# Optimization experiments

Hardware: AMD Instinct MI355X
Metric: run time of the kernel (lower is better)

Reference implementation:

```python
import jax, jax.numpy as jnp
import numpy as np

B, NIMG, H, W, C = 4, 4, 80, 80, 256
NH = 8
C1 = C // 8          # 32
CPH = C1 // NH       # 4 per-head conv channels
K2D = 4              # deformable attention sampling points
HD2 = C1 // NH       # 4 head dim for 2D deformable attention
INNER = 32           # 3D deformable attention inner dim
DSF = (2, 8, 8)
OSC = jnp.array([2.0, 8.0, 8.0], jnp.float32)


def _bilin2d(img, px, py):
    # img [B,C,H,W]; px,py [B,K] pixel coords -> [B,K,C], zero-padded outside
    Bb, Cc, Hh, Ww = img.shape
    x0 = jnp.floor(px); y0 = jnp.floor(py)
    wx = px - x0; wy = py - y0
    bidx = jnp.arange(Bb)[:, None]
    def g(yy, xx):
        valid = (xx >= 0) & (xx <= Ww - 1) & (yy >= 0) & (yy <= Hh - 1)
        xi = jnp.clip(xx, 0, Ww - 1).astype(jnp.int32)
        yi = jnp.clip(yy, 0, Hh - 1).astype(jnp.int32)
        return img[bidx, :, yi, xi] * valid[..., None]
    return (g(y0, x0) * ((1 - wy) * (1 - wx))[..., None]
          + g(y0, x0 + 1) * ((1 - wy) * wx)[..., None]
          + g(y0 + 1, x0) * (wy * (1 - wx))[..., None]
          + g(y0 + 1, x0 + 1) * (wy * wx)[..., None])


def _trilin(img, z, y, x):
    # img [B,C,D,H,W]; z,y,x [B,K] -> [B,K,C]
    Bb, Cc, Dd, Hh, Ww = img.shape
    z0 = jnp.floor(z); y0 = jnp.floor(y); x0 = jnp.floor(x)
    wz = z - z0; wy = y - y0; wx = x - x0
    bidx = jnp.arange(Bb)[:, None]
    def g(zz, yy, xx):
        valid = (zz >= 0) & (zz <= Dd - 1) & (yy >= 0) & (yy <= Hh - 1) & (xx >= 0) & (xx <= Ww - 1)
        zi = jnp.clip(zz, 0, Dd - 1).astype(jnp.int32)
        yi = jnp.clip(yy, 0, Hh - 1).astype(jnp.int32)
        xi = jnp.clip(xx, 0, Ww - 1).astype(jnp.int32)
        return img[bidx, :, zi, yi, xi] * valid[..., None]
    out = 0.
    for dz in (0., 1.):
        for dy in (0., 1.):
            for dx in (0., 1.):
                w = ((1 - wz) if dz == 0. else wz) * ((1 - wy) if dy == 0. else wy) * ((1 - wx) if dx == 0. else wx)
                out = out + g(z0 + dz, y0 + dy, x0 + dx) * w[..., None]
    return out


def _fwd(x, W_qkv, b_qkv, W_fc, b_fc, W_doff, b_doff, W_dep, b_dep, W_st, b_st,
         W_off2d, b_off2d, W_attw, b_attw, W_val, b_val, W_out2d, b_out2d,
         W_q3, b_q3, W_k3, b_k3, W_v3, b_v3, W_offA, b_offA, W_offB, b_offB,
         W_out3, b_out3, rate1, rate2, nimg):
    xb = jnp.transpose(x, (1, 0, 2))                       # [B, nHW, C]
    Bb = xb.shape[0]
    qkv = xb @ W_qkv + b_qkv                               # [B, nHW, 2*C1]
    # ---------- deformable-conv (ACMix) branch ----------
    f_all = qkv.reshape(Bb, nimg * H * W, 2 * NH, CPH).transpose(0, 2, 1, 3)
    f9 = jnp.einsum('oc,bcnk->bonk', W_fc, f_all) + b_fc[None, :, None, None]
    f_conv = f9.transpose(0, 3, 1, 2).reshape(Bb, 9 * CPH, nimg, H, W)
    fin = f_conv.transpose(0, 2, 1, 3, 4).reshape(Bb * nimg, 9 * CPH, H, W)
    off = jax.lax.conv_general_dilated(fin, W_doff, (1, 1), ((1, 1), (1, 1)),
          dimension_numbers=('NCHW', 'OIHW', 'NCHW')) + b_doff[None, :, None, None]
    off = off.reshape(Bb * nimg, 9, 2, H, W)               # (dy,dx) per 3x3 tap
    hh, ww = jnp.meshgrid(jnp.arange(H, dtype=jnp.float32), jnp.arange(W, dtype=jnp.float32), indexing='ij')
    tap = jnp.arange(9)
    ky = (tap // 3 - 1).astype(jnp.float32); kx = (tap % 3 - 1).astype(jnp.float32)
    py = hh[None, None] + ky[None, :, None, None] + off[:, :, 0]
    px = ww[None, None] + kx[None, :, None, None] + off[:, :, 1]
    samp = _bilin2d(fin, px.reshape(Bb * nimg, -1), py.reshape(Bb * nimg, -1))
    samp = samp.reshape(Bb * nimg, 9, H, W, 9 * CPH).transpose(0, 4, 1, 2, 3)
    sg = samp.reshape(Bb * nimg, CPH, 9, 9, H, W)          # [Bn, g, cin_pg, taps, H, W]
    wg = W_dep.reshape(CPH, 27, 9, 9)                      # [g, out_pg, cin_pg, taps]
    dep = jnp.einsum('bgikhw,goik->bgohw', sg, wg).reshape(Bb * nimg, 27 * CPH, H, W) + b_dep[None, :, None, None]
    oc = dep.reshape(Bb, nimg, 27 * CPH, H, W).transpose(0, 2, 1, 3, 4)
    st_in = oc.reshape(Bb, CPH, 27, nimg, H, W)
    st = jnp.einsum('bginhw,goi->bgonhw', st_in, W_st).reshape(Bb, C, nimg, H, W) + b_st[None, :, None, None, None]
    out_conv = st.transpose(2, 3, 4, 0, 1).reshape(nimg * H * W, Bb, C)
    # ---------- per-frame 2D deformable attention ----------
    qk = qkv.reshape(Bb, nimg, H, W, 2, C1)
    q2 = qk[..., 0, :].reshape(Bb * nimg, H, W, C1)
    k2 = qk[..., 1, :].reshape(Bb * nimg, H, W, C1)
    gy, gx = jnp.meshgrid(jnp.arange(H, dtype=jnp.float32) / (H - 1),
                          jnp.arange(W, dtype=jnp.float32) / (W - 1), indexing='ij')
    ref = jnp.stack([gx, gy], -1)                          # [H,W,2] normalized (x,y)
    off2 = (q2 @ W_off2d + b_off2d).reshape(Bb * nimg, H, W, NH, K2D, 2)
    attw = jax.nn.softmax((q2 @ W_attw + b_attw).reshape(Bb * nimg, H, W, NH, K2D), axis=-1)
    v2 = (k2 @ W_val + b_val).reshape(Bb * nimg, H, W, NH, HD2)
    vimg = v2.transpose(0, 3, 4, 1, 2).reshape(Bb * nimg * NH, HD2, H, W)
    loc = ref[None, :, :, None, None, :] + off2 / jnp.array([W, H], jnp.float32)
    ppx = (loc[..., 0] * (W - 1)).transpose(0, 3, 1, 2, 4).reshape(Bb * nimg * NH, H * W * K2D)
    ppy = (loc[..., 1] * (H - 1)).transpose(0, 3, 1, 2, 4).reshape(Bb * nimg * NH, H * W * K2D)
    s2 = _bilin2d(vimg, ppx, ppy).reshape(Bb * nimg, NH, H, W, K2D, HD2)
    a2 = jnp.einsum('bhwnk,bnhwkd->bhwnd', attw, s2).reshape(Bb * nimg, H, W, C1)
    a2 = (a2 @ W_out2d + b_out2d).reshape(Bb, nimg, H, W, C1)
    # faithful reproduction of the source's frame-concat bug: frames [0,0,1,...,nimg-2]
    idx = jnp.array([0] + list(range(nimg - 1)))
    x3 = a2[:, idx].transpose(0, 4, 1, 2, 3)               # [B, C1, nimg, H, W]
    # ---------- 3D deformable attention ----------
    q3 = jnp.einsum('oc,bcnhw->bonhw', W_q3, x3) + b_q3[None, :, None, None, None]
    hid = jax.lax.conv_general_dilated(q3, W_offA, DSF, ((1, 1), (1, 1), (1, 1)),
          dimension_numbers=('NCDHW', 'OIDHW', 'NCDHW')) + b_offA[None, :, None, None, None]
    hid = jax.nn.gelu(hid)
    off3 = jnp.einsum('oc,bcnhw->bonhw', W_offB, hid) + b_offB[None, :, None, None, None]
    off3 = jnp.tanh(off3) * OSC[None, :, None, None, None]
    npr, hpr, wpr = off3.shape[2], off3.shape[3], off3.shape[4]
    gz, gy2, gx2 = jnp.meshgrid(jnp.arange(npr, dtype=jnp.float32) * 2 + 0.5,
                                jnp.arange(hpr, dtype=jnp.float32) * 8 + 3.5,
                                jnp.arange(wpr, dtype=jnp.float32) * 8 + 3.5, indexing='ij')
    cz = (gz[None] + off3[:, 0]).reshape(Bb, -1)
    cy = (gy2[None] + off3[:, 1]).reshape(Bb, -1)
    cx = (gx2[None] + off3[:, 2]).reshape(Bb, -1)
    kf = jnp.einsum('oc,bcnhw->bonhw', W_k3, x3) + b_k3[None, :, None, None, None]
    vf = jnp.einsum('oc,bcnhw->bonhw', W_v3, x3) + b_v3[None, :, None, None, None]
    ks_ = _trilin(kf, cz, cy, cx)                          # [B, L, INNER]
    vs_ = _trilin(vf, cz, cy, cx)
    qf = q3.reshape(Bb, INNER, -1).transpose(0, 2, 1)      # [B, N, INNER]
    at = jax.nn.softmax(jnp.einsum('bnd,bld->bnl', qf, ks_) * (INNER ** -0.5), axis=-1)
    o3 = jnp.einsum('bnl,bld->bnd', at, vs_).transpose(0, 2, 1).reshape(Bb, INNER, nimg, H, W)
    o3 = jnp.einsum('oc,bcnhw->bonhw', W_out3, o3) + b_out3[None, :, None, None, None]
    xattn = o3.transpose(2, 3, 4, 0, 1).reshape(nimg * H * W, Bb, C)
    return rate1 * xattn + rate2 * out_conv


def _p(key, shape, s=0.02):
    return jax.random.normal(key, shape, jnp.float32) * s


def setup_inputs() -> dict:
    key = jax.random.key(0)
    ks = jax.random.split(key, 20)
    z = lambda *s: jnp.zeros(s, jnp.float32)
    return {
        'x': jax.random.normal(ks[0], (NIMG * H * W, B, C), jnp.float32),
        'W_qkv': _p(ks[1], (C, C // 4)), 'b_qkv': z(C // 4),
        'W_fc': _p(ks[2], (9, 2 * NH)), 'b_fc': z(9),
        'W_doff': _p(ks[3], (18, 9 * CPH, 3, 3), 0.01), 'b_doff': z(18),
        'W_dep': _p(ks[4], (27 * CPH, 9, 3, 3)), 'b_dep': z(27 * CPH),
        'W_st': _p(ks[5], (CPH, C // CPH, 27)), 'b_st': z(C),
        'W_off2d': _p(ks[6], (C1, NH * K2D * 2), 0.01), 'b_off2d': z(NH * K2D * 2),
        'W_attw': _p(ks[7], (C1, NH * K2D)), 'b_attw': z(NH * K2D),
        'W_val': _p(ks[8], (C1, C1)), 'b_val': z(C1),
        'W_out2d': _p(ks[9], (C1, C1)), 'b_out2d': z(C1),
        'W_q3': _p(ks[10], (INNER, C1)), 'b_q3': z(INNER),
        'W_k3': _p(ks[11], (INNER, C1)), 'b_k3': z(INNER),
        'W_v3': _p(ks[12], (INNER, C1)), 'b_v3': z(INNER),
        'W_offA': _p(ks[13], (INNER, INNER, 4, 10, 10), 0.01), 'b_offA': z(INNER),
        'W_offB': _p(ks[14], (3, INNER), 0.01), 'b_offB': z(3),
        'W_out3': _p(ks[15], (C, INNER)), 'b_out3': z(C),
        'rate1': jnp.full((1,), 0.5, jnp.float32),
        'rate2': jnp.full((1,), 0.5, jnp.float32),
        'nimg': NIMG,
    }


def reference(x, W_qkv, b_qkv, W_fc, b_fc, W_doff, b_doff, W_dep, b_dep, W_st, b_st,
              W_off2d, b_off2d, W_attw, b_attw, W_val, b_val, W_out2d, b_out2d,
              W_q3, b_q3, W_k3, b_k3, W_v3, b_v3, W_offA, b_offA, W_offB, b_offB,
              W_out3, b_out3, rate1, rate2, nimg):
    return _fwd(x, W_qkv, b_qkv, W_fc, b_fc, W_doff, b_doff, W_dep, b_dep, W_st, b_st,
                W_off2d, b_off2d, W_attw, b_attw, W_val, b_val, W_out2d, b_out2d,
                W_q3, b_q3, W_k3, b_k3, W_v3, b_v3, W_offA, b_offA, W_offB, b_offB,
                W_out3, b_out3, rate1, rate2, nimg)
```

## Files before the change

kernel.cpp:

```cpp
#include <hip/hip_runtime.h>
#include <math.h>

#define B_     4
#define NIMG_  4
#define H_     80
#define W_     80
#define C_     256
#define NH_    8
#define HW_    6400
#define NQ_    25600
#define NPIX_  102400
#define L3_    200

#define WS_QKV 0u
#define WS_Q3  0u
#define WS_KF  3276800u
#define WS_FIN 6553600u
#define WS_A2  6553600u
#define WS_O3  6553600u
#define WS_OFF 10240000u
#define WS_CRD 10240000u
#define WS_KS  10242400u
#define WS_VS  10268000u
#define WS_V2  12083200u
#define WS_VF  12083200u

__global__ __launch_bounds__(256) void k_qkv(const float* __restrict__ x,
        const float* __restrict__ Wq, const float* __restrict__ bq,
        float* __restrict__ qkv) {
    __shared__ __align__(16) float xs[32][256];
    int t = threadIdx.x;
    int row0 = blockIdx.x * 32;
    for (int it = 0; it < 8; ++it) {
        int idx = t + it * 256;
        int r = idx >> 6;
        int f4 = idx & 63;
        int row = row0 + r;
        int b = row / NQ_, n = row % NQ_;
        const float4* src = (const float4*)(x + ((size_t)n * B_ + b) * C_);
        ((float4*)&xs[r][0])[f4] = src[f4];
    }
    __syncthreads();
    int j = t & 63;
    int rbase = (t >> 6) * 8;
    float acc[8];
    #pragma unroll
    for (int r = 0; r < 8; ++r) acc[r] = 0.f;
    for (int c4 = 0; c4 < 64; ++c4) {
        float w0 = Wq[(c4 * 4 + 0) * 64 + j];
        float w1 = Wq[(c4 * 4 + 1) * 64 + j];
        float w2 = Wq[(c4 * 4 + 2) * 64 + j];
        float w3 = Wq[(c4 * 4 + 3) * 64 + j];
        #pragma unroll
        for (int r = 0; r < 8; ++r) {
            float4 xv = ((const float4*)&xs[rbase + r][0])[c4];
            acc[r] += xv.x * w0 + xv.y * w1 + xv.z * w2 + xv.w * w3;
        }
    }
    float bias = bq[j];
    #pragma unroll
    for (int r = 0; r < 8; ++r) {
        int row = row0 + rbase + r;
        qkv[(size_t)row * 64 + j] = acc[r] + bias;
    }
}

__global__ __launch_bounds__(256) void k_fin_v2(const float* __restrict__ qkv,
        const float* __restrict__ Wfc, const float* __restrict__ bfc,
        const float* __restrict__ Wval, const float* __restrict__ bval,
        float* __restrict__ fin, float* __restrict__ v2) {
    __shared__ float WvalL[1024], WfcL[144], bfcL[9], bvalL[32];
    int t = threadIdx.x;
    for (int d = t; d < 1024; d += 256) WvalL[d] = Wval[d];
    if (t < 144) WfcL[t] = Wfc[t];
    if (t >= 160 && t < 169) bfcL[t - 160] = bfc[t - 160];
    if (t >= 192 && t < 224) bvalL[t - 192] = bval[t - 192];
    __syncthreads();
    int P = blockIdx.x * 256 + t;
    int b = P / NQ_, nq = P % NQ_;
    int n = nq / HW_, hw = nq % HW_;
    int bn = b * NIMG_ + n;
    float q[64];
    const float4* qp = (const float4*)(qkv + (size_t)P * 64);
    #pragma unroll
    for (int i = 0; i < 16; ++i) ((float4*)q)[i] = qp[i];
    float fo[36];
    #pragma unroll
    for (int k = 0; k < 4; ++k)
        #pragma unroll
        for (int o = 0; o < 9; ++o) fo[k * 9 + o] = bfcL[o];
    for (int c = 0; c < 16; ++c) {
        #pragma unroll
        for (int o = 0; o < 9; ++o) {
            float wv = WfcL[o * 16 + c];
            #pragma unroll
            for (int k = 0; k < 4; ++k) fo[k * 9 + o] += wv * q[c * 4 + k];
        }
    }
    float* fp = fin + ((size_t)bn * HW_ + hw) * 36;
    #pragma unroll
    for (int i = 0; i < 9; ++i) ((float4*)fp)[i] = ((float4*)fo)[i];
    float vo[32];
    #pragma unroll
    for (int j = 0; j < 32; ++j) vo[j] = bvalL[j];
    for (int c = 0; c < 32; ++c) {
        float qc = q[32 + c];
        #pragma unroll
        for (int j = 0; j < 32; ++j) vo[j] += qc * WvalL[c * 32 + j];
    }
    float* vp = v2 + ((size_t)bn * HW_ + hw) * 32;
    #pragma unroll
    for (int i = 0; i < 8; ++i) ((float4*)vp)[i] = ((float4*)vo)[i];
}

__global__ __launch_bounds__(256) void k_offconv(const float* __restrict__ fin,
        const float* __restrict__ Wdoff, const float* __restrict__ bdoff,
        float* __restrict__ off) {
    __shared__ float Wl[5832];
    int t = threadIdx.x;
    for (int d = t; d < 5832; d += 256) {
        int tap = d / 648, r = d % 648, c = r / 18, o = r % 18;
        Wl[d] = Wdoff[(o * 36 + c) * 9 + tap];
    }
    __syncthreads();
    int P = blockIdx.x * 256 + t;
    int bn = P / HW_, hw = P % HW_;
    int h = hw / W_, w = hw % W_;
    float acc[18];
    #pragma unroll
    for (int o = 0; o < 18; ++o) acc[o] = bdoff[o];
    for (int ky = 0; ky < 3; ++ky) {
        int hh = h + ky - 1;
        if (hh < 0 || hh >= H_) continue;
        for (int kx = 0; kx < 3; ++kx) {
            int ww = w + kx - 1;
            if (ww < 0 || ww >= W_) continue;
            const float* base = fin + ((size_t)bn * HW_ + hh * W_ + ww) * 36;
            const float* wl = Wl + (ky * 3 + kx) * 648;
            #pragma unroll
            for (int c4 = 0; c4 < 9; ++c4) {
                float4 v = ((const float4*)base)[c4];
                const float* w0 = wl + (c4 * 4) * 18;
                #pragma unroll
                for (int o = 0; o < 18; ++o)
                    acc[o] += v.x * w0[o] + v.y * w0[18 + o] + v.z * w0[36 + o] + v.w * w0[54 + o];
            }
        }
    }
    float* op = off + (size_t)P * 18;
    #pragma unroll
    for (int o = 0; o < 18; ++o) op[o] = acc[o];
}

__global__ __launch_bounds__(256, 5) void k_depst(const float* __restrict__ fin,
        const float* __restrict__ off, const float* __restrict__ Wdep,
        const float* __restrict__ bdep, const float* __restrict__ Wst,
        const float* __restrict__ bst, const float* __restrict__ rate2p,
        float* __restrict__ out) {
    __shared__ float wdepL[2187];
    __shared__ float wstL[1728];
    int t = threadIdx.x;
    int g = blockIdx.x & 3;
    for (int d = t; d < 2187; d += 256) {
        int i = d % 9, o = (d / 9) % 27, k = d / 243;
        wdepL[d] = Wdep[(size_t)(g * 27 + o) * 81 + i * 9 + k];
    }
    for (int d = t; d < 1728; d += 256) wstL[d] = Wst[g * 1728 + d];
    __syncthreads();
    int P = (blockIdx.x >> 2) * 256 + t;
    int bn = P / HW_, hw = P % HW_;
    int h = hw / W_, w = hw % W_;
    int b = bn >> 2, n = bn & 3;
    float offs[18];
    const float* offp = off + (size_t)P * 18;
    #pragma unroll
    for (int i = 0; i < 18; ++i) offs[i] = offp[i];
    const float* finb = fin + (size_t)bn * HW_ * 36 + g * 9;
    float acc[27];
    #pragma unroll
    for (int o = 0; o < 27; ++o) acc[o] = 0.f;
    #pragma unroll 1
    for (int k = 0; k < 9; ++k) {
        float py = (float)h + (float)(k / 3 - 1) + offs[k * 2 + 0];
        float px = (float)w + (float)(k % 3 - 1) + offs[k * 2 + 1];
        float y0 = floorf(py), x0 = floorf(px);
        float wy = py - y0, wx = px - x0;
        float s[9];
        #pragma unroll
        for (int i = 0; i < 9; ++i) s[i] = 0.f;
        #pragma unroll 1
        for (int cy = 0; cy < 2; ++cy) {
            float yf = y0 + (float)cy;
            if (yf < 0.f || yf > 79.f) continue;
            float wyf = cy ? wy : 1.f - wy;
            int yi = (int)yf;
            #pragma unroll 1
            for (int cx = 0; cx < 2; ++cx) {
                float xf = x0 + (float)cx;
                if (xf < 0.f || xf > 79.f) continue;
                float wgt = wyf * (cx ? wx : 1.f - wx);
                int xi = (int)xf;
                const float* cp = finb + ((size_t)yi * W_ + xi) * 36;
                #pragma unroll
                for (int i = 0; i < 9; ++i) s[i] += wgt * cp[i];
            }
        }
        const float* wd = wdepL + k * 243;
        #pragma unroll
        for (int o = 0; o < 27; ++o) {
            float tmp = 0.f;
            #pragma unroll
            for (int i = 0; i < 9; ++i) tmp += s[i] * wd[o * 9 + i];
            acc[o] += tmp;
        }
    }
    #pragma unroll
    for (int i = 0; i < 27; ++i) acc[i] += bdep[g * 27 + i];
    float r2 = rate2p[0];
    float* ob = out + ((size_t)(n * HW_ + hw) * B_ + b) * C_ + g * 64;
    #pragma unroll 1
    for (int o4 = 0; o4 < 16; ++o4) {
        float res[4];
        #pragma unroll
        for (int qq = 0; qq < 4; ++qq) {
            int o = o4 * 4 + qq;
            float a = bst[g * 64 + o];
            #pragma unroll
            for (int i = 0; i < 27; ++i) a += acc[i] * wstL[o * 27 + i];
            res[qq] = r2 * a;
        }
        ((float4*)ob)[o4] = make_float4(res[0], res[1], res[2], res[3]);
    }
}

__global__ __launch_bounds__(256) void k_attn2d(const float* __restrict__ qkv,
        const float* __restrict__ v2,
        const float* __restrict__ Woff, const float* __restrict__ boff,
        const float* __restrict__ Watt, const float* __restrict__ batt,
        const float* __restrict__ Wout, const float* __restrict__ bout,
        float* __restrict__ a2) {
    __shared__ float WoffL[2048], WattL[1024], WoutL[1024];
    __shared__ float boffL[64], battL[32], boutL[32];
    int t = threadIdx.x;
    for (int d = t; d < 2048; d += 256) WoffL[d] = Woff[d];
    for (int d = t; d < 1024; d += 256) { WattL[d] = Watt[d]; WoutL[d] = Wout[d]; }
    if (t < 64) boffL[t] = boff[t];
    else if (t < 96) battL[t - 64] = batt[t - 64];
    else if (t < 128) boutL[t - 96] = bout[t - 96];
    __syncthreads();
    int P = blockIdx.x * 256 + t;
    int b = P / NQ_, nq = P % NQ_;
    int n = nq / HW_, hw = nq % HW_;
    int h = hw / W_, w = hw % W_;
    int bn = b * NIMG_ + n;
    float q[32];
    const float4* qp = (const float4*)(qkv + (size_t)P * 64);
    #pragma unroll
    for (int i = 0; i < 8; ++i) ((float4*)q)[i] = qp[i];
    const float* vbase = v2 + (size_t)bn * HW_ * 32;
    float a2v[32];
    #pragma unroll
    for (int i = 0; i < 32; ++i) a2v[i] = 0.f;
    for (int nh = 0; nh < 8; ++nh) {
        float t0 = battL[nh * 4 + 0], t1 = battL[nh * 4 + 1];
        float t2 = battL[nh * 4 + 2], t3 = battL[nh * 4 + 3];
        for (int c = 0; c < 32; ++c) {
            float qc = q[c];
            const float* wr = WattL + c * 32 + nh * 4;
            t0 += qc * wr[0]; t1 += qc * wr[1]; t2 += qc * wr[2]; t3 += qc * wr[3];
        }
        float m = fmaxf(fmaxf(t0, t1), fmaxf(t2, t3));
        float e0 = expf(t0 - m), e1 = expf(t1 - m), e2 = expf(t2 - m), e3 = expf(t3 - m);
        float inv = 1.f / (e0 + e1 + e2 + e3);
        float pk[4] = {e0 * inv, e1 * inv, e2 * inv, e3 * inv};
        #pragma unroll
        for (int kk = 0; kk < 4; ++kk) {
            int j0 = nh * 8 + kk * 2;
            float ox = boffL[j0], oy = boffL[j0 + 1];
            for (int c = 0; c < 32; ++c) {
                float qc = q[c];
                ox += qc * WoffL[c * 64 + j0];
                oy += qc * WoffL[c * 64 + j0 + 1];
            }
            float ppx = (float)w + ox * (79.f / 80.f);
            float ppy = (float)h + oy * (79.f / 80.f);
            float x0 = floorf(ppx), y0 = floorf(ppy);
            float wx = ppx - x0, wy = ppy - y0;
            float s0 = 0.f, s1 = 0.f, s2 = 0.f, s3 = 0.f;
            #pragma unroll
            for (int cy = 0; cy < 2; ++cy) {
                float yf = y0 + (float)cy;
                if (yf < 0.f || yf > 79.f) continue;
                float wyf = cy ? wy : 1.f - wy;
                int yi = (int)yf;
                #pragma unroll
                for (int cx = 0; cx < 2; ++cx) {
                    float xf = x0 + (float)cx;
                    if (xf < 0.f || xf > 79.f) continue;
                    float wgt = wyf * (cx ? wx : 1.f - wx);
                    int xi = (int)xf;
                    float4 vv = *(const float4*)(vbase + ((size_t)yi * W_ + xi) * 32 + nh * 4);
                    s0 += wgt * vv.x; s1 += wgt * vv.y; s2 += wgt * vv.z; s3 += wgt * vv.w;
                }
            }
            float p = pk[kk];
            a2v[nh * 4 + 0] += p * s0; a2v[nh * 4 + 1] += p * s1;
            a2v[nh * 4 + 2] += p * s2; a2v[nh * 4 + 3] += p * s3;
        }
    }
    float ro[32];
    #pragma unroll
    for (int o = 0; o < 32; ++o) ro[o] = boutL[o];
    for (int c = 0; c < 32; ++c) {
        float ac = a2v[c];
        const float* wr = WoutL + c * 32;
        #pragma unroll
        for (int o = 0; o < 32; ++o) ro[o] += ac * wr[o];
    }
    float* op = a2 + ((size_t)bn * HW_ + hw) * 32;
    #pragma unroll
    for (int i = 0; i < 8; ++i) ((float4*)op)[i] = ((float4*)ro)[i];
}

__global__ __launch_bounds__(256) void k_qkv3(const float* __restrict__ a2,
        const float* __restrict__ Wq3, const float* __restrict__ bq3,
        const float* __restrict__ Wk3, const float* __restrict__ bk3,
        const float* __restrict__ Wv3, const float* __restrict__ bv3,
        float* __restrict__ q3, float* __restrict__ kf, float* __restrict__ vf) {
    __shared__ float Wq3L[1024], Wk3L[1024], Wv3L[1024];
    __shared__ float bq3L[32], bk3L[32], bv3L[32];
    int t = threadIdx.x;
    for (int d = t; d < 1024; d += 256) {
        Wq3L[d] = Wq3[d]; Wk3L[d] = Wk3[d]; Wv3L[d] = Wv3[d];
    }
    if (t < 32) { bq3L[t] = bq3[t]; bk3L[t] = bk3[t]; bv3L[t] = bv3[t]; }
    __syncthreads();
    int idx = blockIdx.x * 256 + t;
    int bn = idx / HW_, hw = idx % HW_;
    int b = bn >> 2, n = bn & 3;
    int ns = (n == 0) ? 0 : n - 1;
    const float* src = a2 + ((size_t)(b * 4 + ns) * HW_ + hw) * 32;
    float v[32];
    #pragma unroll
    for (int i = 0; i < 8; ++i) ((float4*)v)[i] = ((const float4*)src)[i];
    float oq[32], ok[32], ov[32];
    #pragma unroll
    for (int o = 0; o < 32; ++o) {
        float aq = bq3L[o], ak = bk3L[o], av = bv3L[o];
        #pragma unroll
        for (int c = 0; c < 32; ++c) {
            aq += Wq3L[o * 32 + c] * v[c];
            ak += Wk3L[o * 32 + c] * v[c];
            av += Wv3L[o * 32 + c] * v[c];
        }
        oq[o] = aq; ok[o] = ak; ov[o] = av;
    }
    float* qo = q3 + (size_t)idx * 32;
    float* ko = kf + (size_t)idx * 32;
    float* vo = vf + (size_t)idx * 32;
    #pragma unroll
    for (int i = 0; i < 8; ++i) {
        ((float4*)qo)[i] = ((float4*)oq)[i];
        ((float4*)ko)[i] = ((float4*)ok)[i];
        ((float4*)vo)[i] = ((float4*)ov)[i];
    }
}

__global__ __launch_bounds__(256) void k_offs3d(const float* __restrict__ q3,
        const float* __restrict__ WoffA, const float* __restrict__ boffA,
        const float* __restrict__ WoffB, const float* __restrict__ boffB,
        float* __restrict__ coords) {
    __shared__ float red[4][128];
    __shared__ float hidl[128];
    int t = threadIdx.x;
    int blk = blockIdx.x;
    int zo = blk / 100, r = blk % 100, ho = r / 10, wo = r % 10;
    float acc[4][32];
    #pragma unroll
    for (int b = 0; b < 4; ++b)
        #pragma unroll
        for (int o = 0; o < 32; ++o) acc[b][o] = 0.f;
    for (int tap = t; tap < 400; tap += 256) {
        int kz = tap / 100, r2 = tap % 100, ky = r2 / 10, kx = r2 % 10;
        int zi = zo * 2 + kz - 1, hi = ho * 8 + ky - 1, wi = wo * 8 + kx - 1;
        if (zi < 0 || zi >= NIMG_ || hi < 0 || hi >= H_ || wi < 0 || wi >= W_) continue;
        const float* wb = WoffA + tap;
        int sp = hi * W_ + wi;
        for (int c = 0; c < 32; ++c) {
            float vb[4];
            #pragma unroll
            for (int b = 0; b < 4; ++b)
                vb[b] = q3[((size_t)(b * 4 + zi) * HW_ + sp) * 32 + c];
            #pragma unroll
            for (int o = 0; o < 32; ++o) {
                float wv = wb[(o * 32 + c) * 400];
                #pragma unroll
                for (int b = 0; b < 4; ++b) acc[b][o] += vb[b] * wv;
            }
        }
    }
    #pragma unroll
    for (int b = 0; b < 4; ++b)
        #pragma unroll
        for (int o = 0; o < 32; ++o)
            for (int sh = 32; sh >= 1; sh >>= 1)
                acc[b][o] += __shfl_xor(acc[b][o], sh);
    int lane = t & 63, wv = t >> 6;
    if (lane == 0)
        for (int b = 0; b < 4; ++b)
            for (int o = 0; o < 32; ++o) red[wv][b * 32 + o] = acc[b][o];
    __syncthreads();
    if (t < 128) {
        float v = red[0][t] + red[1][t] + red[2][t] + red[3][t] + boffA[t & 31];
        float v3 = v * v * v;
        hidl[t] = 0.5f * v * (1.f + tanhf(0.7978845608028654f * (v + 0.044715f * v3)));
    }
    __syncthreads();
    if (t < 12) {
        int b = t / 3, j = t % 3;
        float a = boffB[j];
        for (int o = 0; o < 32; ++o) a += WoffB[j * 32 + o] * hidl[b * 32 + o];
        float osc = (j == 0) ? 2.f : 8.f;
        float base = (j == 0) ? (zo * 2 + 0.5f) : ((j == 1) ? (ho * 8 + 3.5f) : (wo * 8 + 3.5f));
        coords[((size_t)b * L3_ + blk) * 3 + j] = base + tanhf(a) * osc;
    }
}

__global__ __launch_bounds__(256) void k_trisample(const float* __restrict__ kf,
        const float* __restrict__ vf, const float* __restrict__ coords,
        float* __restrict__ ks, float* __restrict__ vs) {
    int t = threadIdx.x;
    int wv = blockIdx.x * 4 + (t >> 6);
    int b = wv / L3_, l = wv % L3_;
    int lane = t & 63;
    int c = lane & 31;
    const float* src = (lane < 32) ? kf : vf;
    float* dst = (lane < 32) ? ks : vs;
    const float* cp = coords + ((size_t)b * L3_ + l) * 3;
    float cz = cp[0], cy = cp[1], cx = cp[2];
    float z0 = floorf(cz), y0 = floorf(cy), x0 = floorf(cx);
    float wz = cz - z0, wy = cy - y0, wx = cx - x0;
    float acc = 0.f;
    #pragma unroll
    for (int dz = 0; dz < 2; ++dz) {
        float zf = z0 + (float)dz;
        if (zf < 0.f || zf > 3.f) continue;
        float wzf = dz ? wz : 1.f - wz;
        int zi = (int)zf;
        #pragma unroll
        for (int dy = 0; dy < 2; ++dy) {
            float yf = y0 + (float)dy;
            if (yf < 0.f || yf > 79.f) continue;
            float wyf = wzf * (dy ? wy : 1.f - wy);
            int yi = (int)yf;
            #pragma unroll
            for (int dx = 0; dx < 2; ++dx) {
                float xf = x0 + (float)dx;
                if (xf < 0.f || xf > 79.f) continue;
                float wgt = wyf * (dx ? wx : 1.f - wx);
                int xi = (int)xf;
                acc += wgt * src[((size_t)(b * 4 + zi) * HW_ + yi * W_ + xi) * 32 + c];
            }
        }
    }
    dst[((size_t)b * L3_ + l) * 32 + c] = acc;
}

__global__ __launch_bounds__(256) void k_attn3d(const float* __restrict__ q3,
        const float* __restrict__ ks, const float* __restrict__ vs,
        float* __restrict__ o3) {
    __shared__ __align__(16) float ksl[L3_ * 32];
    __shared__ __align__(16) float vsl[L3_ * 32];
    int t = threadIdx.x;
    int b = blockIdx.x / 100;
    int chunk = blockIdx.x % 100;
    const float4* ksg = (const float4*)(ks + (size_t)b * L3_ * 32);
    const float4* vsg = (const float4*)(vs + (size_t)b * L3_ * 32);
    for (int d = t; d < L3_ * 8; d += 256) {
        ((float4*)ksl)[d] = ksg[d];
        ((float4*)vsl)[d] = vsg[d];
    }
    __syncthreads();
    int N = chunk * 256 + t;
    float q[32];
    const float4* qp = (const float4*)(q3 + ((size_t)b * NQ_ + N) * 32);
    #pragma unroll
    for (int i = 0; i < 8; ++i) ((float4*)q)[i] = qp[i];
    const float scale = 0.17677669529663687f;
    float den = 0.f;
    float o[32];
    #pragma unroll
    for (int c = 0; c < 32; ++c) o[c] = 0.f;
    for (int l = 0; l < L3_; ++l) {
        const float4* kp = (const float4*)(ksl + l * 32);
        float s = 0.f;
        #pragma unroll
        for (int c4 = 0; c4 < 8; ++c4) {
            float4 kv = kp[c4];
            s += q[c4 * 4 + 0] * kv.x + q[c4 * 4 + 1] * kv.y + q[c4 * 4 + 2] * kv.z + q[c4 * 4 + 3] * kv.w;
        }
        float p = expf(s * scale);
        den += p;
        const float4* vp = (const float4*)(vsl + l * 32);
        #pragma unroll
        for (int c4 = 0; c4 < 8; ++c4) {
            float4 vv = vp[c4];
            o[c4 * 4 + 0] += p * vv.x; o[c4 * 4 + 1] += p * vv.y;
            o[c4 * 4 + 2] += p * vv.z; o[c4 * 4 + 3] += p * vv.w;
        }
    }
    float inv = 1.f / den;
    float* op = o3 + ((size_t)b * NQ_ + N) * 32;
    #pragma unroll
    for (int c = 0; c < 32; ++c) op[c] = o[c] * inv;
}

__global__ __launch_bounds__(256) void k_final(const float* __restrict__ o3,
        const float* __restrict__ W, const float* __restrict__ bias,
        const float* __restrict__ r1p, float* __restrict__ out) {
    __shared__ float o3T[32 * 128];
    __shared__ float WT[32 * 260];
    int t = threadIdx.x;
    int R0 = blockIdx.x * 128;
    {
        int row = t >> 1, k0 = (t & 1) * 16;
        int R = R0 + row;
        int b = R & 3, N = R >> 2;
        const float* src = o3 + ((size_t)b * NQ_ + N) * 32 + k0;
        #pragma unroll
        for (int j = 0; j < 16; ++j) o3T[(k0 + j) * 128 + row] = src[j];
    }
    for (int d = t; d < 8192; d += 256) {
        int c = d >> 5, k = d & 31;
        WT[k * 260 + c] = W[d];
    }
    __syncthreads();
    int tc = t & 15;
    int tr = t >> 4;
    int r0 = tr * 8;
    float acc[8][16];
    #pragma unroll
    for (int i = 0; i < 8; ++i)
        #pragma unroll
        for (int j = 0; j < 16; ++j) acc[i][j] = 0.f;
    #pragma unroll 1
    for (int k = 0; k < 32; ++k) {
        float a[8];
        *(float4*)&a[0] = *(const float4*)&o3T[k * 128 + r0];
        *(float4*)&a[4] = *(const float4*)&o3T[k * 128 + r0 + 4];
        float wv[16];
        #pragma unroll
        for (int ci = 0; ci < 16; ++ci) wv[ci] = WT[k * 260 + tc + 16 * ci];
        #pragma unroll
        for (int i = 0; i < 8; ++i)
            #pragma unroll
            for (int j = 0; j < 16; ++j) acc[i][j] += a[i] * wv[j];
    }
    float r1 = r1p[0];
    float bs[16];
    #pragma unroll
    for (int ci = 0; ci < 16; ++ci) bs[ci] = bias[tc + 16 * ci];
    #pragma unroll 1
    for (int i = 0; i < 8; ++i) {
        size_t rowbase = (size_t)(R0 + r0 + i) * 256;
        #pragma unroll
        for (int j = 0; j < 16; ++j) {
            size_t oi = rowbase + tc + 16 * j;
            out[oi] = r1 * (acc[i][j] + bs[j]) + out[oi];
        }
    }
}

extern "C" void kernel_launch(void* const* d_in, const int* in_sizes, int n_in,
                              void* d_out, int out_size, void* d_ws, size_t ws_size,
                              hipStream_t stream) {
    (void)in_sizes; (void)n_in; (void)out_size; (void)ws_size;
    const float* x      = (const float*)d_in[0];
    const float* W_qkv  = (const float*)d_in[1];
    const float* b_qkv  = (const float*)d_in[2];
    const float* W_fc   = (const float*)d_in[3];
    const float* b_fc   = (const float*)d_in[4];
    const float* W_doff = (const float*)d_in[5];
    const float* b_doff = (const float*)d_in[6];
    const float* W_dep  = (const float*)d_in[7];
    const float* b_dep  = (const float*)d_in[8];
    const float* W_st   = (const float*)d_in[9];
    const float* b_st   = (const float*)d_in[10];
    const float* W_off2d= (const float*)d_in[11];
    const float* b_off2d= (const float*)d_in[12];
    const float* W_attw = (const float*)d_in[13];
    const float* b_attw = (const float*)d_in[14];
    const float* W_val  = (const float*)d_in[15];
    const float* b_val  = (const float*)d_in[16];
    const float* W_out2d= (const float*)d_in[17];
    const float* b_out2d= (const float*)d_in[18];
    const float* W_q3   = (const float*)d_in[19];
    const float* b_q3   = (const float*)d_in[20];
    const float* W_k3   = (const float*)d_in[21];
    const float* b_k3   = (const float*)d_in[22];
    const float* W_v3   = (const float*)d_in[23];
    const float* b_v3   = (const float*)d_in[24];
    const float* W_offA = (const float*)d_in[25];
    const float* b_offA = (const float*)d_in[26];
    const float* W_offB = (const float*)d_in[27];
    const float* b_offB = (const float*)d_in[28];
    const float* W_out3 = (const float*)d_in[29];
    const float* b_out3 = (const float*)d_in[30];
    const float* rate1  = (const float*)d_in[31];
    const float* rate2  = (const float*)d_in[32];

    float* ws  = (float*)d_ws;
    float* out = (float*)d_out;
    float* qkv = ws + WS_QKV;
    float* fin = ws + WS_FIN;
    float* off = ws + WS_OFF;
    float* v2  = ws + WS_V2;
    float* a2  = ws + WS_A2;
    float* q3  = ws + WS_Q3;
    float* kf  = ws + WS_KF;
    float* vf  = ws + WS_VF;
    float* crd = ws + WS_CRD;
    float* ks  = ws + WS_KS;
    float* vs  = ws + WS_VS;
    float* o3w = ws + WS_O3;

    k_qkv      <<<3200,   256, 0, stream>>>(x, W_qkv, b_qkv, qkv);
    k_fin_v2   <<<400,    256, 0, stream>>>(qkv, W_fc, b_fc, W_val, b_val, fin, v2);
    k_offconv  <<<400,    256, 0, stream>>>(fin, W_doff, b_doff, off);
    k_depst    <<<1600,   256, 0, stream>>>(fin, off, W_dep, b_dep, W_st, b_st, rate2, out);
    k_attn2d   <<<400,    256, 0, stream>>>(qkv, v2, W_off2d, b_off2d, W_attw, b_attw, W_out2d, b_out2d, a2);
    k_qkv3     <<<400,    256, 0, stream>>>(a2, W_q3, b_q3, W_k3, b_k3, W_v3, b_v3, q3, kf, vf);
    k_offs3d   <<<200,    256, 0, stream>>>(q3, W_offA, b_offA, W_offB, b_offB, crd);
    k_trisample<<<200,    256, 0, stream>>>(kf, vf, crd, ks, vs);
    k_attn3d   <<<400,    256, 0, stream>>>(q3, ks, vs, o3w);
    k_final    <<<800,    256, 0, stream>>>(o3w, W_out3, b_out3, rate1, out);
}
```

Before: 962.4 us.

## Restructure deformable conv kernel: all groups per block, shared offsets, branchless bilinear

The depthwise-deformable plus strided conv kernel now processes all four channel groups of 128 pixels in one 512-thread block. Adjacent threads handle different groups of the same pixel, so fin gathers and output writes coalesce better, and the offsets are loaded once per block into shared memory. Bilinear sampling is made branchless with clamped indices and validity weights, which removes divergence at the cost of always doing four loads. The block order is remapped with a stride of 100. The larger per-block LDS footprint, about 73KB, holding all groups' weights, may limit occupancy.

```diff
diff --git a/kernel.cpp b/kernel.cpp
--- a/kernel.cpp
+++ b/kernel.cpp
@@ -152,60 +152,72 @@
     for (int o = 0; o < 18; ++o) op[o] = acc[o];
 }
 
-__global__ __launch_bounds__(256, 5) void k_depst(const float* __restrict__ fin,
+__global__ __launch_bounds__(512, 4) void k_depst(const float* __restrict__ fin,
         const float* __restrict__ off, const float* __restrict__ Wdep,
         const float* __restrict__ bdep, const float* __restrict__ Wst,
         const float* __restrict__ bst, const float* __restrict__ rate2p,
         float* __restrict__ out) {
-    __shared__ float wdepL[2187];
-    __shared__ float wstL[1728];
-    int t = threadIdx.x;
-    int g = blockIdx.x & 3;
-    for (int d = t; d < 2187; d += 256) {
-        int i = d % 9, o = (d / 9) % 27, k = d / 243;
-        wdepL[d] = Wdep[(size_t)(g * 27 + o) * 81 + i * 9 + k];
-    }
-    for (int d = t; d < 1728; d += 256) wstL[d] = Wst[g * 1728 + d];
-    __syncthreads();
-    int P = (blockIdx.x >> 2) * 256 + t;
+    __shared__ float wdepL[8748];
+    __shared__ float wstL[6928];
+    __shared__ float offL[2304];
+    __shared__ float bdepL[108];
+    __shared__ float bstL[256];
+    int t = threadIdx.x;
+    int bx = blockIdx.x;
+    int pb = (bx & 7) * 100 + (bx >> 3);
+    int P0 = pb * 128;
+    for (int d = t; d < 8748; d += 512) {
+        int i = d % 9, o = (d / 9) % 27, k = (d / 243) % 9, g2 = d / 2187;
+        wdepL[d] = Wdep[(size_t)(g2 * 27 + o) * 81 + i * 9 + k];
+    }
+    for (int d = t; d < 6912; d += 512) {
+        int g2 = d / 1728, r = d % 1728;
+        wstL[g2 * 1732 + r] = Wst[d];
+    }
+    for (int d = t; d < 2304; d += 512) offL[d] = off[(size_t)P0 * 18 + d];
+    if (t < 108) bdepL[t] = bdep[t];
+    if (t < 256) bstL[t] = bst[t];
+    __syncthreads();
+    int g = t & 3, ploc = t >> 2;
+    int P = P0 + ploc;
     int bn = P / HW_, hw = P % HW_;
     int h = hw / W_, w = hw % W_;
     int b = bn >> 2, n = bn & 3;
-    float offs[18];
-    const float* offp = off + (size_t)P * 18;
-    #pragma unroll
-    for (int i = 0; i < 18; ++i) offs[i] = offp[i];
     const float* finb = fin + (size_t)bn * HW_ * 36 + g * 9;
+    const float* wdg = wdepL + g * 2187;
+    const float* wsg = wstL + g * 1732;
     float acc[27];
     #pragma unroll
     for (int o = 0; o < 27; ++o) acc[o] = 0.f;
+    float hf = (float)h, wf = (float)w;
     #pragma unroll 1
     for (int k = 0; k < 9; ++k) {
-        float py = (float)h + (float)(k / 3 - 1) + offs[k * 2 + 0];
-        float px = (float)w + (float)(k % 3 - 1) + offs[k * 2 + 1];
-        float y0 = floorf(py), x0 = floorf(px);
-        float wy = py - y0, wx = px - x0;
+        float py = hf + (float)(k / 3 - 1) + offL[ploc * 18 + k * 2 + 0];
+        float px = wf + (float)(k % 3 - 1) + offL[ploc * 18 + k * 2 + 1];
+        float y0f = floorf(py), x0f = floorf(px);
+        float wy = py - y0f, wx = px - x0f;
+        float wy0 = 1.f - wy, wx0 = 1.f - wx;
+        float vy0 = (y0f >= 0.f && y0f <= 79.f) ? 1.f : 0.f;
+        float vy1 = (y0f >= -1.f && y0f <= 78.f) ? 1.f : 0.f;
+        float vx0 = (x0f >= 0.f && x0f <= 79.f) ? 1.f : 0.f;
+        float vx1 = (x0f >= -1.f && x0f <= 78.f) ? 1.f : 0.f;
+        int yi0 = (int)fminf(fmaxf(y0f, 0.f), 79.f);
+        int yi1 = (int)fminf(fmaxf(y0f + 1.f, 0.f), 79.f);
+        int xi0 = (int)fminf(fmaxf(x0f, 0.f), 79.f);
+        int xi1 = (int)fminf(fmaxf(x0f + 1.f, 0.f), 79.f);
+        float w00 = wy0 * wx0 * vy0 * vx0;
+        float w01 = wy0 * wx  * vy0 * vx1;
+        float w10 = wy  * wx0 * vy1 * vx0;
+        float w11 = wy  * wx  * vy1 * vx1;
+        const float* c00 = finb + ((size_t)(yi0 * W_ + xi0)) * 36;
+        const float* c01 = finb + ((size_t)(yi0 * W_ + xi1)) * 36;
+        const float* c10 = finb + ((size_t)(yi1 * W_ + xi0)) * 36;
+        const float* c11 = finb + ((size_t)(yi1 * W_ + xi1)) * 36;
         float s[9];
         #pragma unroll
-        for (int i = 0; i < 9; ++i) s[i] = 0.f;
-        #pragma unroll 1
-        for (int cy = 0; cy < 2; ++cy) {
-            float yf = y0 + (float)cy;
-            if (yf < 0.f || yf > 79.f) continue;
-            float wyf = cy ? wy : 1.f - wy;
-            int yi = (int)yf;
-            #pragma unroll 1
-            for (int cx = 0; cx < 2; ++cx) {
-                float xf = x0 + (float)cx;
-                if (xf < 0.f || xf > 79.f) continue;
-                float wgt = wyf * (cx ? wx : 1.f - wx);
-                int xi = (int)xf;
-                const float* cp = finb + ((size_t)yi * W_ + xi) * 36;
-                #pragma unroll
-                for (int i = 0; i < 9; ++i) s[i] += wgt * cp[i];
-            }
-        }
-        const float* wd = wdepL + k * 243;
+        for (int i = 0; i < 9; ++i)
+            s[i] = w00 * c00[i] + w01 * c01[i] + w10 * c10[i] + w11 * c11[i];
+        const float* wd = wdg + k * 243;
         #pragma unroll
         for (int o = 0; o < 27; ++o) {
             float tmp = 0.f;
@@ -215,7 +227,7 @@
         }
     }
     #pragma unroll
-    for (int i = 0; i < 27; ++i) acc[i] += bdep[g * 27 + i];
+    for (int i = 0; i < 27; ++i) acc[i] += bdepL[g * 27 + i];
     float r2 = rate2p[0];
     float* ob = out + ((size_t)(n * HW_ + hw) * B_ + b) * C_ + g * 64;
     #pragma unroll 1
@@ -224,9 +236,9 @@
         #pragma unroll
         for (int qq = 0; qq < 4; ++qq) {
             int o = o4 * 4 + qq;
-            float a = bst[g * 64 + o];
-            #pragma unroll
-            for (int i = 0; i < 27; ++i) a += acc[i] * wstL[o * 27 + i];
+            float a = bstL[g * 64 + o];
+            #pragma unroll
+            for (int i = 0; i < 27; ++i) a += acc[i] * wsg[o * 27 + i];
             res[qq] = r2 * a;
         }
         ((float4*)ob)[o4] = make_float4(res[0], res[1], res[2], res[3]);
@@ -627,7 +639,7 @@
     k_qkv      <<<3200,   256, 0, stream>>>(x, W_qkv, b_qkv, qkv);
     k_fin_v2   <<<400,    256, 0, stream>>>(qkv, W_fc, b_fc, W_val, b_val, fin, v2);
     k_offconv  <<<400,    256, 0, stream>>>(fin, W_doff, b_doff, off);
-    k_depst    <<<1600,   256, 0, stream>>>(fin, off, W_dep, b_dep, W_st, b_st, rate2, out);
+    k_depst    <<<800,    512, 0, stream>>>(fin, off, W_dep, b_dep, W_st, b_st, rate2, out);
     k_attn2d   <<<400,    256, 0, stream>>>(qkv, v2, W_off2d, b_off2d, W_attw, b_attw, W_out2d, b_out2d, a2);
     k_qkv3     <<<400,    256, 0, stream>>>(a2, W_q3, b_q3, W_k3, b_k3, W_v3, b_v3, q3, kf, vf);
     k_offs3d   <<<200,    256, 0, stream>>>(q3, W_offA, b_offA, W_offB, b_offB, crd);
```

Measured after the change: 915.8 us. 4.8% less time.
